# Performance work log

Measured on AMD Instinct MI355X. Metric: run time of the kernel, lower is better.

## Reference

```python
import jax, jax.numpy as jnp
import numpy as np

B, D, L, K = 4096, 1024, 16384, 64


def setup_inputs() -> dict:
    key = jax.random.key(0)
    k1, k2, k3, k4, k5 = jax.random.split(key, 5)
    x = jax.random.normal(k1, (B, D), dtype=jnp.float32)
    # torch nn.Linear weights are [out_features, in_features]
    W_enc = jax.random.normal(k2, (L, D), dtype=jnp.float32) * (1.0 / np.sqrt(D))
    b_enc = jax.random.normal(k3, (L,), dtype=jnp.float32) * 0.01
    W_dec = jax.random.normal(k4, (D, L), dtype=jnp.float32) * (1.0 / np.sqrt(L))
    b_dec = jax.random.normal(k5, (D,), dtype=jnp.float32) * 0.01
    return {"x": x, "W_enc": W_enc, "b_enc": b_enc, "W_dec": W_dec, "b_dec": b_dec}


def reference(x, W_enc, b_enc, W_dec, b_dec):
    # xbar = x - decoder.bias
    xbar = x - b_dec                                   # [B, D]
    a = jnp.einsum('bd,ld->bl', xbar, W_enc) + b_enc   # [B, L]
    vals, idx = jax.lax.top_k(a, K)                    # [B, K]
    f = jnp.zeros_like(a)
    rows = jnp.arange(a.shape[0])[:, None]             # [B, 1]
    f = f.at[rows, idx].set(jax.nn.relu(vals))         # sparse latent [B, L]
    xhat = jnp.einsum('bl,dl->bd', f, W_dec) + b_dec   # [B, D]
    return (f, xhat)
```

## Files before the change

### kernel.cpp

```cpp
#include <hip/hip_runtime.h>

#define B_N 4096
#define D_N 1024
#define L_N 16384
#define K_N 64
#define CAP 512
#define CNT_STRIDE 16

typedef __attribute__((ext_vector_type(8))) short bf16x8;
typedef __attribute__((ext_vector_type(4))) float f32x4;

__device__ __forceinline__ unsigned short f2bf(float f) {
  union { float f; unsigned int u; } v; v.f = f;
  unsigned int r = v.u + 0x7FFFu + ((v.u >> 16) & 1u);
  return (unsigned short)(r >> 16);
}
__device__ __forceinline__ float bf2f(unsigned short u) {
  union { unsigned int u; float f; } v; v.u = (unsigned int)u << 16;
  return v.f;
}

__global__ __launch_bounds__(256) void prep_all(const float* __restrict__ x,
                                                const float* __restrict__ W_enc,
                                                const float* __restrict__ W_dec,
                                                const float* __restrict__ b_dec,
                                                unsigned short* __restrict__ wencb,
                                                unsigned short* __restrict__ xbarb,
                                                float* __restrict__ srow,
                                                unsigned short* __restrict__ WdTb,
                                                int* __restrict__ cand_cnt) {
  __shared__ float tile[32][33];
  __shared__ float wsum[4];
  const int t = threadIdx.x;
  const int bid = blockIdx.x;
  if (bid < 16384) {
    size_t i = (size_t)bid * 256 + t;
    float4 v = ((const float4*)W_enc)[i];
    ushort4 o;
    o.x = f2bf(v.x); o.y = f2bf(v.y); o.z = f2bf(v.z); o.w = f2bf(v.w);
    ((ushort4*)wencb)[i] = o;
  } else if (bid < 20480) {
    const int b = bid - 16384;
    if (t == 0) cand_cnt[b * CNT_STRIDE] = 0;
    float4 v = ((const float4*)x)[(size_t)b * 256 + t];
    float4 bd = ((const float4*)b_dec)[t];
    float4 e = make_float4(v.x - bd.x, v.y - bd.y, v.z - bd.z, v.w - bd.w);
    ushort4 o;
    o.x = f2bf(e.x); o.y = f2bf(e.y); o.z = f2bf(e.z); o.w = f2bf(e.w);
    ((ushort4*)xbarb)[(size_t)b * 256 + t] = o;
    float ss = e.x * e.x + e.y * e.y + e.z * e.z + e.w * e.w;
#pragma unroll
    for (int off = 32; off; off >>= 1) ss += __shfl_down(ss, off);
    if ((t & 63) == 0) wsum[t >> 6] = ss;
    __syncthreads();
    if (t == 0) srow[b] = sqrtf((wsum[0] + wsum[1] + wsum[2] + wsum[3]) * (1.0f / D_N));
  } else {
    const int tb = bid - 20480;
    const int l0 = (tb & 511) * 32;
    const int d0 = (tb >> 9) * 32;
    const int tx = t & 31, ty = t >> 5;
    for (int i = ty; i < 32; i += 8)
      tile[i][tx] = W_dec[(size_t)(d0 + i) * L_N + l0 + tx];
    __syncthreads();
    for (int i = ty; i < 32; i += 8)
      WdTb[(size_t)(l0 + i) * D_N + d0 + tx] = f2bf(tile[tx][i]);
  }
}

__global__ __launch_bounds__(512, 2) void gemm_enc_select(
    const unsigned short* __restrict__ A,
    const unsigned short* __restrict__ Bw,
    const float* __restrict__ b_enc,
    const float* __restrict__ srow,
    int* __restrict__ cand_cnt,
    float* __restrict__ cand_val,
    int* __restrict__ cand_idx,
    float* __restrict__ f) {
  __shared__ __align__(16) char smem[131072];
  const int tid = threadIdx.x;
  const int wid = tid >> 6, lane = tid & 63;
  const int wm = wid >> 2, wn = wid & 3;
  const int fr = lane & 15, quad = lane >> 4;

  const int wg = ((blockIdx.x & 7) << 7) + (blockIdx.x >> 3);
  const int bm = wg & 15, bn = wg >> 4;

  const int stgrow = wid * 8 + (lane >> 3);
  const int scol = ((lane & 7) ^ (lane >> 3)) << 4;
  const char* gA = (const char*)A + ((size_t)(bm * 256 + stgrow) * D_N) * 2 + scol;
  const char* gB = (const char*)Bw + ((size_t)(bn * 256 + stgrow) * D_N) * 2 + scol;

#define STAGE(kt_, p_)                                                                     \
  {                                                                                        \
    const size_t ko_ = (size_t)(kt_)*128;                                                  \
    _Pragma("unroll") for (int r_ = 0; r_ < 4; ++r_) {                                     \
      __builtin_amdgcn_global_load_lds(                                                    \
          (const __attribute__((address_space(1))) void*)(gA + (size_t)r_ * 131072 + ko_), \
          (__attribute__((address_space(3))) void*)(smem + (p_) * 65536 + r_ * 8192 + wid * 1024), \
          16, 0, 0);                                                                       \
      __builtin_amdgcn_global_load_lds(                                                    \
          (const __attribute__((address_space(1))) void*)(gB + (size_t)r_ * 131072 + ko_), \
          (__attribute__((address_space(3))) void*)(smem + (p_) * 65536 + 32768 + r_ * 8192 + wid * 1024), \
          16, 0, 0);                                                                       \
    }                                                                                      \
  }

  f32x4 acc[8][4];
#pragma unroll
  for (int i = 0; i < 8; ++i)
#pragma unroll
    for (int j = 0; j < 4; ++j) acc[i][j] = (f32x4){0.f, 0.f, 0.f, 0.f};

  const int aB = (wm * 128 + fr) * 128;
  const int bB = 32768 + (wn * 64 + fr) * 128;
  const int s0 = (quad ^ (fr & 7)) << 4;

  STAGE(0, 0);
  __syncthreads();

  for (int kt = 0; kt < D_N / 64; ++kt) {
    const int pb = (kt & 1) * 65536;
    if (kt < D_N / 64 - 1) STAGE(kt + 1, (kt & 1) ^ 1);

#pragma unroll
    for (int ks = 0; ks < 2; ++ks) {
      bf16x8 af[8], bv[4];
#pragma unroll
      for (int i = 0; i < 8; ++i)
        af[i] = *(const bf16x8*)(smem + pb + aB + i * 2048 + (s0 ^ (ks * 64)));
#pragma unroll
      for (int j = 0; j < 4; ++j)
        bv[j] = *(const bf16x8*)(smem + pb + bB + j * 2048 + (s0 ^ (ks * 64)));
#pragma unroll
      for (int i = 0; i < 8; ++i)
#pragma unroll
        for (int j = 0; j < 4; ++j)
          acc[i][j] = __builtin_amdgcn_mfma_f32_16x16x32_bf16(af[i], bv[j], acc[i][j], 0, 0, 0);
    }

    __syncthreads();
  }

  const int lc0 = bn * 256 + wn * 64 + fr;
  float be[4];
#pragma unroll
  for (int nj = 0; nj < 4; ++nj) be[nj] = b_enc[lc0 + nj * 16];
  const int gr0 = bm * 256 + wm * 128 + quad * 4;
#pragma unroll
  for (int mi = 0; mi < 8; ++mi) {
#pragma unroll
    for (int r = 0; r < 4; ++r) {
      const int grow = gr0 + mi * 16 + r;
      const float thr = 2.3f * srow[grow];
#pragma unroll
      for (int nj = 0; nj < 4; ++nj) {
        const float val = acc[mi][nj][r] + be[nj];
        if (val > thr) {
          const int p = atomicAdd(&cand_cnt[grow * CNT_STRIDE], 1);
          if (p < CAP) {
            cand_val[(size_t)grow * CAP + p] = val;
            cand_idx[(size_t)grow * CAP + p] = lc0 + nj * 16;
          }
        }
      }
    }
  }

  {
    const float4 z4 = make_float4(0.f, 0.f, 0.f, 0.f);
    float4* fz = (float4*)(f + (size_t)(bm * 256) * L_N + bn * 256);
#pragma unroll
    for (int it = 0; it < 32; ++it) {
      const int idx = it * 512 + tid;
      const int rr = idx >> 6, cc = idx & 63;
      fz[(size_t)rr * (L_N / 4) + cc] = z4;
    }
  }
#undef STAGE
}

__global__ __launch_bounds__(256) void select_decode(
    const float* __restrict__ x,
    const float* __restrict__ W_enc,
    const float* __restrict__ b_enc,
    const float* __restrict__ b_dec,
    const float* __restrict__ srow,
    const int* __restrict__ cand_cnt,
    const float* __restrict__ cand_val,
    const int* __restrict__ cand_idx,
    const unsigned short* __restrict__ WdTb,
    float* __restrict__ f,
    float* __restrict__ xhat) {
  const int b = blockIdx.x, t = threadIdx.x;
  const int lane = t & 63, wave = t >> 6;
  __shared__ double xd[D_N];
  __shared__ float cv[CAP];
  __shared__ int ci[CAP];
  __shared__ double bu[128];
  __shared__ int bidx[128];
  __shared__ int o_idx[K_N];
  __shared__ float o_val[K_N];
  __shared__ int sidx[K_N];
  __shared__ float sval[K_N];
  __shared__ int nb_s, nin_s, outcnt;
  __shared__ float v64_s;

  const int cnt = min(cand_cnt[b * CNT_STRIDE], CAP);
  if (t == 0) { nb_s = 0; nin_s = 0; outcnt = 0; v64_s = -1e30f; }
  for (int c = t; c < cnt; c += 256) {
    cv[c] = cand_val[(size_t)b * CAP + c];
    ci[c] = cand_idx[(size_t)b * CAP + c];
  }
  for (int i = t; i < D_N; i += 256)
    xd[i] = (double)x[(size_t)b * D_N + i] - (double)b_dec[i];
  __syncthreads();

  for (int c = t; c < cnt; c += 256) {
    const float v = cv[c];
    const int id = ci[c];
    int r = 0;
    for (int k = 0; k < cnt; ++k)
      r += (cv[k] > v || (cv[k] == v && ci[k] < id)) ? 1 : 0;
    if (r == 63) v64_s = v;
  }
  __syncthreads();
  const float v64 = v64_s;
  const float m = 0.04f * srow[b];

  for (int c = t; c < cnt; c += 256) {
    const float v = cv[c];
    if (v > v64 + m) {
      atomicAdd(&nin_s, 1);
    } else if (v >= v64 - m) {
      const int p = atomicAdd(&nb_s, 1);
      if (p < 128) bidx[p] = c;
    }
  }
  __syncthreads();
  const int nb = min(nb_s, 128);
  const int nin = nin_s;
  int nneed = K_N - nin;
  if (nneed < 0) nneed = 0;

  for (int c = wave; c < nb; c += 4) {
    const int l = ci[bidx[c]];
    const float4* wr = (const float4*)(W_enc + (size_t)l * D_N);
    double acc = 0.0;
#pragma unroll
    for (int j = 0; j < 4; ++j) {
      float4 w4 = wr[j * 64 + lane];
      const int base = (j * 64 + lane) * 4;
      acc += xd[base + 0] * (double)w4.x + xd[base + 1] * (double)w4.y +
             xd[base + 2] * (double)w4.z + xd[base + 3] * (double)w4.w;
    }
#pragma unroll
    for (int off = 32; off; off >>= 1) acc += __shfl_down(acc, off);
    if (lane == 0) bu[c] = acc + (double)b_enc[l];
  }
  __syncthreads();

  for (int c = t; c < cnt; c += 256) {
    if (cv[c] > v64 + m) {
      const int p = atomicAdd(&outcnt, 1);
      if (p < K_N) { o_idx[p] = ci[c]; o_val[p] = cv[c]; }
    }
  }
  if (t < nb) {
    const double uv = bu[t];
    const int l = ci[bidx[t]];
    int r = 0;
    for (int k = 0; k < nb; ++k)
      r += (bu[k] > uv || (bu[k] == uv && ci[bidx[k]] < l)) ? 1 : 0;
    if (r < nneed) {
      const int p = atomicAdd(&outcnt, 1);
      if (p < K_N) { o_idx[p] = l; o_val[p] = (float)uv; }
    }
  }
  __syncthreads();
  const int ns = min(outcnt, K_N);

  if (t < K_N) {
    sidx[t] = (t < ns) ? o_idx[t] : t;
    sval[t] = (t < ns) ? fmaxf(o_val[t], 0.0f) : 0.0f;
  }
  __syncthreads();

  if (t < ns) f[(size_t)b * L_N + sidx[t]] = sval[t];

  float4 acc = ((const float4*)b_dec)[t];
#pragma unroll 8
  for (int k = 0; k < K_N; ++k) {
    const float v = sval[k];
    const ushort4 w = ((const ushort4*)(WdTb + (size_t)sidx[k] * D_N))[t];
    acc.x += v * bf2f(w.x); acc.y += v * bf2f(w.y);
    acc.z += v * bf2f(w.z); acc.w += v * bf2f(w.w);
  }
  ((float4*)(xhat + (size_t)b * D_N))[t] = acc;
}

extern "C" void kernel_launch(void* const* d_in, const int* in_sizes, int n_in,
                              void* d_out, int out_size, void* d_ws, size_t ws_size,
                              hipStream_t stream) {
  (void)in_sizes; (void)n_in; (void)out_size; (void)ws_size;
  const float* x     = (const float*)d_in[0];
  const float* W_enc = (const float*)d_in[1];
  const float* b_enc = (const float*)d_in[2];
  const float* W_dec = (const float*)d_in[3];
  const float* b_dec = (const float*)d_in[4];

  float* f    = (float*)d_out;
  float* xhat = (float*)d_out + (size_t)B_N * L_N;

  char* ws = (char*)d_ws;
  unsigned short* wencb = (unsigned short*)ws;
  unsigned short* xbarb = (unsigned short*)(ws + 33554432);
  unsigned short* WdTb  = (unsigned short*)(ws + 41943040);
  float* srow           = (float*)(ws + 75497472);
  int* cand_cnt         = (int*)(ws + 75513856);
  float* cand_val       = (float*)(ws + 75776000);
  int* cand_idx         = (int*)(ws + 84164608);

  prep_all<<<36864, 256, 0, stream>>>(x, W_enc, W_dec, b_dec, wencb, xbarb, srow,
                                      WdTb, cand_cnt);
  gemm_enc_select<<<1024, 512, 0, stream>>>(
      xbarb, wencb, b_enc, srow, cand_cnt, cand_val, cand_idx, f);
  select_decode<<<B_N, 256, 0, stream>>>(x, W_enc, b_enc, b_dec, srow,
                                         cand_cnt, cand_val, cand_idx, WdTb, f, xhat);
}
```

Before: 812.6 us.

## Interleave encoder GEMM loads and MFMAs in fine-grained phases with explicit waitcnts

Restructures the encoder GEMM main loop into four sub-phases per K-tile. Each phase issues half of the next tile's global-to-LDS loads, reads LDS fragments for half the rows, and runs 16 MFMAs at raised wave priority. Explicit barriers and vmcnt/lgkmcnt waits replace the coarse per-tile __syncthreads. The wave-to-row mapping is changed so that each 128-row half of the block tile is split across the two wm waves, and the epilogue row indexing is updated to match. The goal is to overlap memory traffic with matrix math and lower register pressure, at the cost of many more barriers and fragile hand-tuned wait counts.

New measurement: 803.7 us. No clear change (-1.1%).

```diff
diff --git a/kernel.cpp b/kernel.cpp
--- a/kernel.cpp
+++ b/kernel.cpp
@@ -90,20 +90,36 @@
   const char* gA = (const char*)A + ((size_t)(bm * 256 + stgrow) * D_N) * 2 + scol;
   const char* gB = (const char*)Bw + ((size_t)(bn * 256 + stgrow) * D_N) * 2 + scol;
 
-#define STAGE(kt_, p_)                                                                     \
-  {                                                                                        \
-    const size_t ko_ = (size_t)(kt_)*128;                                                  \
-    _Pragma("unroll") for (int r_ = 0; r_ < 4; ++r_) {                                     \
-      __builtin_amdgcn_global_load_lds(                                                    \
-          (const __attribute__((address_space(1))) void*)(gA + (size_t)r_ * 131072 + ko_), \
-          (__attribute__((address_space(3))) void*)(smem + (p_) * 65536 + r_ * 8192 + wid * 1024), \
-          16, 0, 0);                                                                       \
-      __builtin_amdgcn_global_load_lds(                                                    \
-          (const __attribute__((address_space(1))) void*)(gB + (size_t)r_ * 131072 + ko_), \
-          (__attribute__((address_space(3))) void*)(smem + (p_) * 65536 + 32768 + r_ * 8192 + wid * 1024), \
-          16, 0, 0);                                                                       \
-    }                                                                                      \
-  }
+#define STG(gsrc_, doff_, r0_, po_, ko_)                                                   \
+  _Pragma("unroll") for (int r_ = (r0_); r_ < (r0_) + 2; ++r_) {                           \
+    __builtin_amdgcn_global_load_lds(                                                      \
+        (const __attribute__((address_space(1))) void*)((gsrc_) + (size_t)r_ * 131072 + (ko_)), \
+        (__attribute__((address_space(3))) void*)(smem + (po_) + (doff_) + r_ * 8192 + wid * 1024), \
+        16, 0, 0);                                                                         \
+  }
+
+#define DSRD(rh_, ks_)                                                                     \
+  bf16x8 af[4], bv[4];                                                                     \
+  _Pragma("unroll") for (int i_ = 0; i_ < 4; ++i_)                                         \
+      af[i_] = *(const bf16x8*)(smem + pb + (rh_)*16384 + aB + i_ * 2048 + (s0 ^ ((ks_)*64))); \
+  _Pragma("unroll") for (int j_ = 0; j_ < 4; ++j_)                                         \
+      bv[j_] = *(const bf16x8*)(smem + pb + bB + j_ * 2048 + (s0 ^ ((ks_)*64)));
+
+#define MFMA16(rh_)                                                                        \
+  __builtin_amdgcn_s_setprio(1);                                                           \
+  _Pragma("unroll") for (int i_ = 0; i_ < 4; ++i_)                                         \
+      _Pragma("unroll") for (int j_ = 0; j_ < 4; ++j_)                                     \
+          acc[(rh_)*4 + i_][j_] = __builtin_amdgcn_mfma_f32_16x16x32_bf16(                 \
+              af[i_], bv[j_], acc[(rh_)*4 + i_][j_], 0, 0, 0);                             \
+  __builtin_amdgcn_s_setprio(0);
+
+#define BAR __builtin_amdgcn_s_barrier()
+#define LGKM0                                                                              \
+  do {                                                                                     \
+    asm volatile("s_waitcnt lgkmcnt(0)" ::: "memory");                                     \
+    __builtin_amdgcn_sched_barrier(0);                                                     \
+  } while (0)
+#define VMW(n_) asm volatile("s_waitcnt vmcnt(" #n_ ")" ::: "memory")
 
   f32x4 acc[8][4];
 #pragma unroll
@@ -111,46 +127,43 @@
 #pragma unroll
     for (int j = 0; j < 4; ++j) acc[i][j] = (f32x4){0.f, 0.f, 0.f, 0.f};
 
-  const int aB = (wm * 128 + fr) * 128;
+  const int aB = (wm * 64 + fr) * 128;
   const int bB = 32768 + (wn * 64 + fr) * 128;
   const int s0 = (quad ^ (fr & 7)) << 4;
 
-  STAGE(0, 0);
-  __syncthreads();
-
-  for (int kt = 0; kt < D_N / 64; ++kt) {
+  STG(gB, 32768, 0, 0, (size_t)0)
+  STG(gB, 32768, 2, 0, (size_t)0)
+  STG(gA, 0, 0, 0, (size_t)0)
+  STG(gA, 0, 2, 0, (size_t)0)
+  VMW(2);
+  BAR;
+
+  for (int kt = 0; kt < 15; ++kt) {
     const int pb = (kt & 1) * 65536;
-    if (kt < D_N / 64 - 1) STAGE(kt + 1, (kt & 1) ^ 1);
-
-#pragma unroll
-    for (int ks = 0; ks < 2; ++ks) {
-      bf16x8 af[8], bv[4];
-#pragma unroll
-      for (int i = 0; i < 8; ++i)
-        af[i] = *(const bf16x8*)(smem + pb + aB + i * 2048 + (s0 ^ (ks * 64)));
-#pragma unroll
-      for (int j = 0; j < 4; ++j)
-        bv[j] = *(const bf16x8*)(smem + pb + bB + j * 2048 + (s0 ^ (ks * 64)));
-#pragma unroll
-      for (int i = 0; i < 8; ++i)
-#pragma unroll
-        for (int j = 0; j < 4; ++j)
-          acc[i][j] = __builtin_amdgcn_mfma_f32_16x16x32_bf16(af[i], bv[j], acc[i][j], 0, 0, 0);
-    }
-
-    __syncthreads();
+    const int po = pb ^ 65536;
+    const size_t ko = (size_t)(kt + 1) * 128;
+    { DSRD(0, 0) STG(gB, 32768, 0, po, ko) BAR; LGKM0; MFMA16(0) BAR; }
+    { DSRD(0, 1) STG(gB, 32768, 2, po, ko) BAR; LGKM0; MFMA16(0) VMW(4); BAR; }
+    { DSRD(1, 0) STG(gA, 0, 0, po, ko) BAR; LGKM0; MFMA16(1) BAR; }
+    { DSRD(1, 1) STG(gA, 0, 2, po, ko) BAR; LGKM0; MFMA16(1) VMW(2); BAR; }
+  }
+  {
+    const int pb = 65536;
+    { DSRD(0, 0) BAR; LGKM0; MFMA16(0) BAR; }
+    { DSRD(0, 1) BAR; LGKM0; MFMA16(0) VMW(0); BAR; }
+    { DSRD(1, 0) BAR; LGKM0; MFMA16(1) BAR; }
+    { DSRD(1, 1) BAR; LGKM0; MFMA16(1) }
   }
 
   const int lc0 = bn * 256 + wn * 64 + fr;
   float be[4];
 #pragma unroll
   for (int nj = 0; nj < 4; ++nj) be[nj] = b_enc[lc0 + nj * 16];
-  const int gr0 = bm * 256 + wm * 128 + quad * 4;
 #pragma unroll
   for (int mi = 0; mi < 8; ++mi) {
 #pragma unroll
     for (int r = 0; r < 4; ++r) {
-      const int grow = gr0 + mi * 16 + r;
+      const int grow = bm * 256 + (mi >> 2) * 128 + wm * 64 + (mi & 3) * 16 + quad * 4 + r;
       const float thr = 2.3f * srow[grow];
 #pragma unroll
       for (int nj = 0; nj < 4; ++nj) {
@@ -176,7 +189,12 @@
       fz[(size_t)rr * (L_N / 4) + cc] = z4;
     }
   }
-#undef STAGE
+#undef STG
+#undef DSRD
+#undef MFMA16
+#undef BAR
+#undef LGKM0
+#undef VMW
 }
 
 __global__ __launch_bounds__(256) void select_decode(
```
